# Kernel tuning notes

Measured on AMD Instinct MI355X. Metric: run time of the kernel, lower is better.

The kernel has to match this reference:

```python
import jax, jax.numpy as jnp
import numpy as np


def setup_inputs() -> dict:
    key = jax.random.key(0)
    k1, k2, k3, k4 = jax.random.split(key, 4)
    B, S, E, H = 8, 2048, 4096, 128  # batch, seq, embed, head_size
    scale = 1.0 / np.sqrt(E)
    return {
        "x": jax.random.normal(k1, (B, S, E), dtype=jnp.float32),
        "Wq": jax.random.normal(k2, (E, H), dtype=jnp.float32) * scale,
        "Wk": jax.random.normal(k3, (E, H), dtype=jnp.float32) * scale,
        "Wv": jax.random.normal(k4, (E, H), dtype=jnp.float32) * scale,
    }


def reference(x, Wq, Wk, Wv):
    # Single-head attention, non-flash branch, mask=None, eval-mode dropout.
    q = jnp.einsum("bse,eh->bsh", x, Wq)  # [B,S,H]
    k = jnp.einsum("bse,eh->bsh", x, Wk)
    v = jnp.einsum("bse,eh->bsh", x, Wv)
    head_size = k.shape[-1]
    scores = jnp.einsum("bqh,bkh->bqk", q, k) * (head_size ** -0.5)  # [B,S,S]
    attn = jax.nn.softmax(scores, axis=-1)
    out = jnp.einsum("bqk,bkh->bqh", attn, v)  # [B,S,H]
    return out
```

## Files before the change

### kernel.cpp

```cpp
#include <hip/hip_runtime.h>
#include <math.h>

typedef __bf16 bf16_t;
typedef bf16_t bf16x8 __attribute__((ext_vector_type(8)));
typedef float floatx4 __attribute__((ext_vector_type(4)));

#define MFMA(a, b, c) __builtin_amdgcn_mfma_f32_16x16x32_bf16(a, b, c, 0, 0, 0)

static constexpr int S = 2048, E = 4096, H = 128;

__device__ __forceinline__ void gl_lds16(const void* g, void* l) {
  __builtin_amdgcn_global_load_lds((const __attribute__((address_space(1))) void*)g,
                                   (__attribute__((address_space(3))) void*)l,
                                   16, 0, 0);
}

__global__ __launch_bounds__(256) void wt_kernel(const float* __restrict__ Wq,
                                                 const float* __restrict__ Wk,
                                                 const float* __restrict__ Wv,
                                                 bf16_t* __restrict__ Wt) {
  __shared__ bf16_t tile[64][130];
  int wb = blockIdx.x / 64;
  int eb = blockIdx.x % 64;
  const float* W = wb == 0 ? Wq : (wb == 1 ? Wk : Wv);
  int t = threadIdx.x;
  {
    int er = t >> 2, q = t & 3;
    const float4* src = (const float4*)(W + (size_t)(eb * 64 + er) * H + q * 32);
    for (int i = 0; i < 8; ++i) {
      float4 f = src[i];
      int c = q * 32 + i * 4;
      tile[er][c + 0] = (bf16_t)f.x; tile[er][c + 1] = (bf16_t)f.y;
      tile[er][c + 2] = (bf16_t)f.z; tile[er][c + 3] = (bf16_t)f.w;
    }
  }
  __syncthreads();
  {
    int h = t >> 1, half = t & 1;
    bf16_t buf[32];
    for (int j = 0; j < 32; ++j) buf[j] = tile[half * 32 + j][h];
    bf16_t* dst = Wt + (size_t)(wb * H + h) * E + eb * 64 + half * 32;
    for (int i = 0; i < 4; ++i) ((uint4*)dst)[i] = ((uint4*)buf)[i];
  }
}

__global__ __launch_bounds__(512, 2) void qkv_kernel(const float* __restrict__ X,
                                                     const bf16_t* __restrict__ Wt,
                                                     bf16_t* __restrict__ Qb,
                                                     bf16_t* __restrict__ Kb,
                                                     bf16_t* __restrict__ Vt) {
  __shared__ __align__(16) char smem[114688];
  constexpr int B0X = 0, B0W = 8192, B1X = 57344, B1W = 65536;

  int mBase = blockIdx.x * 64;
  int t = threadIdx.x, lane = t & 63, w = t >> 6;
  int r16 = lane & 15, q4 = lane >> 4;

  floatx4 acc[4][3] = {};

  int xrow = t >> 3;
  const float* xbase = X + (size_t)(mBase + xrow) * E + (t & 7) * 4;
  int wrl = lane >> 3, wg = lane & 7;

  floatx4 xo[2], xe[2];

#define FENCE() asm volatile("" ::: "memory")
#define WAITB(N)                                                                 \
  do {                                                                           \
    asm volatile("s_waitcnt vmcnt(" #N ") lgkmcnt(0)" ::: "memory");             \
    __builtin_amdgcn_s_barrier();                                                \
    asm volatile("" ::: "memory");                                               \
  } while (0)

#define LOAD_X(XR, K0)                                                           \
  _Pragma("unroll") for (int i = 0; i < 2; ++i)                                  \
      (XR)[i] = __builtin_nontemporal_load(                                      \
          (const floatx4*)(xbase + (K0) + i * 32));

#define STAGE_W(WOFF, K0)                                                        \
  _Pragma("unroll") for (int is = 0; is < 6; ++is) {                             \
    int row = w * 48 + is * 8 + wrl;                                             \
    int g = wg ^ (row & 7);                                                      \
    gl_lds16(Wt + (size_t)row * E + (K0) + g * 8,                                \
             smem + (WOFF) + (w * 48 + is * 8) * 128 + lane * 16);               \
  }

#define STAGE_X(XOFF, XR)                                                        \
  _Pragma("unroll") for (int i = 0; i < 2; ++i) {                                \
    floatx4 f = (XR)[i];                                                         \
    bf16_t pk[4] = {(bf16_t)f[0], (bf16_t)f[1], (bf16_t)f[2], (bf16_t)f[3]};     \
    int gc = ((t & 7) >> 1) + i * 4;                                             \
    int g = gc ^ (xrow & 7);                                                     \
    *(uint2*)(smem + (XOFF) + xrow * 128 + g * 16 + (t & 1) * 8) = *(uint2*)pk;  \
  }

#define COMPUTE(XOFF, WOFF)                                                      \
  __builtin_amdgcn_s_setprio(1);                                                 \
  _Pragma("unroll") for (int kc = 0; kc < 2; ++kc) {                             \
    bf16x8 a[4], b[3];                                                           \
    _Pragma("unroll") for (int i = 0; i < 4; ++i) {                              \
      int row = i * 16 + r16;                                                    \
      int sl = (kc * 4 + q4) ^ (row & 7);                                        \
      a[i] = *(const bf16x8*)(smem + (XOFF) + row * 128 + sl * 16);              \
    }                                                                            \
    _Pragma("unroll") for (int j = 0; j < 3; ++j) {                              \
      int row = w * 48 + j * 16 + r16;                                           \
      int sl = (kc * 4 + q4) ^ (row & 7);                                        \
      b[j] = *(const bf16x8*)(smem + (WOFF) + row * 128 + sl * 16);              \
    }                                                                            \
    _Pragma("unroll") for (int i = 0; i < 4; ++i)                                \
        _Pragma("unroll") for (int j = 0; j < 3; ++j)                            \
            acc[i][j] = MFMA(a[i], b[j], acc[i][j]);                             \
  }                                                                              \
  __builtin_amdgcn_s_setprio(0);

  LOAD_X(xe, 0);
  FENCE();
  STAGE_W(B0W, 0);
  FENCE();
  STAGE_X(B0X, xe);
  FENCE();
  LOAD_X(xo, 64);
  LOAD_X(xe, 128);
  WAITB(4);

  for (int kb = 0; kb < 62; kb += 2) {
    STAGE_W(B1W, (kb + 1) * 64);
    FENCE();
    STAGE_X(B1X, xo);
    FENCE();
    LOAD_X(xo, (kb + 3) * 64);
    FENCE();
    COMPUTE(B0X, B0W);
    WAITB(2);

    STAGE_W(B0W, (kb + 2) * 64);
    FENCE();
    STAGE_X(B0X, xe);
    FENCE();
    if (kb < 60) {
      LOAD_X(xe, (kb + 4) * 64);
      FENCE();
      COMPUTE(B1X, B1W);
      WAITB(2);
    } else {
      COMPUTE(B1X, B1W);
      WAITB(0);
    }
  }
  STAGE_W(B1W, 63 * 64);
  FENCE();
  STAGE_X(B1X, xo);
  FENCE();
  COMPUTE(B0X, B0W);
  WAITB(0);
  COMPUTE(B1X, B1W);

  int bb = mBase >> 11, sBase = mBase & 2047;
  bf16_t(*Ob)[264] = (bf16_t(*)[264])smem;
#pragma unroll
  for (int i = 0; i < 4; ++i)
#pragma unroll
    for (int j = 0; j < 3; ++j) {
      int ncol = w * 48 + j * 16;
      if (ncol >= 256) {
        int h = ncol - 256 + r16;
        bf16_t pk[4];
#pragma unroll
        for (int ii = 0; ii < 4; ++ii) pk[ii] = (bf16_t)acc[i][j][ii];
        *(uint2*)&Vt[((size_t)bb * H + h) * S + sBase + i * 16 + q4 * 4] =
            *(uint2*)pk;
      } else {
#pragma unroll
        for (int ii = 0; ii < 4; ++ii)
          Ob[i * 16 + q4 * 4 + ii][ncol + r16] = (bf16_t)acc[i][j][ii];
      }
    }
  __syncthreads();
  {
    int row = t >> 3, g = t & 7;
    bf16_t* qp = Qb + (size_t)(mBase + row) * H + g * 16;
    bf16_t* kp = Kb + (size_t)(mBase + row) * H + g * 16;
    *(uint4*)qp = *(uint4*)&Ob[row][g * 16];
    *(uint4*)(qp + 8) = *(uint4*)&Ob[row][g * 16 + 8];
    *(uint4*)kp = *(uint4*)&Ob[row][128 + g * 16];
    *(uint4*)(kp + 8) = *(uint4*)&Ob[row][128 + g * 16 + 8];
  }
#undef LOAD_X
#undef STAGE_W
#undef STAGE_X
#undef COMPUTE
#undef FENCE
#undef WAITB
}

__global__ __launch_bounds__(256, 2) void attn_kernel(const bf16_t* __restrict__ Qb,
                                                      const bf16_t* __restrict__ Kb,
                                                      const bf16_t* __restrict__ Vt,
                                                      float* __restrict__ Op,
                                                      float* __restrict__ Mp,
                                                      float* __restrict__ Lp) {
  __shared__ __align__(16) char smem[74752];

  int bid = blockIdx.x;
  int b = bid & 7, r = bid >> 3;
  int qt = r >> 1, half = r & 1;

  int t = threadIdx.x, lane = t & 63, wl = t >> 6;
  int r16 = lane & 15, q4 = lane >> 4;
  bf16_t(*Pl)[72] = (bf16_t(*)[72])(smem + 65536 + wl * 2304);

  bf16x8 qf[4];
  {
    const bf16_t* qp = Qb + (size_t)(b * S + qt * 64 + wl * 16 + r16) * H + q4 * 8;
#pragma unroll
    for (int c = 0; c < 4; ++c) qf[c] = *(const bf16x8*)(qp + c * 32);
  }
  bf16x8 onef;
#pragma unroll
  for (int i = 0; i < 8; ++i) onef[i] = (bf16_t)1.0f;

  floatx4 o[8] = {};
  float m_r[4], l_r[4];
#pragma unroll
  for (int ii = 0; ii < 4; ++ii) { m_r[ii] = -1e30f; l_r[ii] = 0.f; }
  const float scale = 0.08838834764831845f;

  int kr = lane >> 4, kg = lane & 15;
  int vr = lane >> 3, vg = lane & 7;

#define STAGE_KV(BUF, KT)                                                        \
  _Pragma("unroll") for (int is = 0; is < 4; ++is) {                             \
    int row = wl * 16 + is * 4 + kr;                                             \
    int g = kg ^ (row & 15);                                                     \
    gl_lds16(Kb + (size_t)(b * S + (KT) * 64 + row) * H + g * 8,                 \
             smem + (BUF) + (wl * 16 + is * 4) * 256 + lane * 16);               \
  }                                                                              \
  _Pragma("unroll") for (int is = 0; is < 4; ++is) {                             \
    int row = wl * 32 + is * 8 + vr;                                             \
    int g = vg ^ (row & 7);                                                      \
    gl_lds16(Vt + (size_t)(b * H + row) * S + (KT) * 64 + g * 8,                 \
             smem + (BUF) + 16384 + (wl * 32 + is * 8) * 128 + lane * 16);       \
  }

  STAGE_KV(0, half * 16);
  __syncthreads();

  for (int it = 0; it < 16; ++it) {
    int cur = (it & 1) << 15;
    if (it < 15) { STAGE_KV(cur ^ 32768, half * 16 + it + 1); }
    const char* kbase = smem + cur;
    bf16_t(*Vl)[64] = (bf16_t(*)[64])(smem + cur + 16384);

    floatx4 s4[4] = {};
    __builtin_amdgcn_s_setprio(1);
#pragma unroll
    for (int c = 0; c < 4; ++c)
#pragma unroll
      for (int j = 0; j < 4; ++j) {
        int row = j * 16 + r16;
        int sl = (c * 4 + q4) ^ r16;
        bf16x8 bk = *(const bf16x8*)(kbase + row * 256 + sl * 16);
        s4[j] = MFMA(qf[c], bk, s4[j]);
      }
    __builtin_amdgcn_s_setprio(0);

    float p[4][4], mxl[4];
#pragma unroll
    for (int ii = 0; ii < 4; ++ii) mxl[ii] = -1e30f;
#pragma unroll
    for (int j = 0; j < 4; ++j)
#pragma unroll
      for (int ii = 0; ii < 4; ++ii) {
        float sv = s4[j][ii] * scale;
        p[j][ii] = sv;
        mxl[ii] = fmaxf(mxl[ii], sv);
      }
    int ok = 1;
#pragma unroll
    for (int ii = 0; ii < 4; ++ii) ok &= (mxl[ii] <= m_r[ii] + 8.f) ? 1 : 0;
    if (!__all(ok)) {
      float alpha[4];
#pragma unroll
      for (int off = 1; off <= 8; off <<= 1)
#pragma unroll
        for (int ii = 0; ii < 4; ++ii)
          mxl[ii] = fmaxf(mxl[ii], __shfl_xor(mxl[ii], off));
#pragma unroll
      for (int ii = 0; ii < 4; ++ii) {
        float mn = fmaxf(m_r[ii], mxl[ii]);
        alpha[ii] = __expf(m_r[ii] - mn);
        m_r[ii] = mn;
        l_r[ii] *= alpha[ii];
      }
#pragma unroll
      for (int f = 0; f < 8; ++f)
#pragma unroll
        for (int ii = 0; ii < 4; ++ii) o[f][ii] *= alpha[ii];
    }
#pragma unroll
    for (int j = 0; j < 4; ++j)
#pragma unroll
      for (int ii = 0; ii < 4; ++ii) {
        float e = __expf(p[j][ii] - m_r[ii]);
        Pl[q4 * 4 + ii][j * 16 + r16] = (bf16_t)e;
      }

    bf16x8 pa0 = *(const bf16x8*)&Pl[r16][q4 * 8];
    bf16x8 pa1 = *(const bf16x8*)&Pl[r16][32 + q4 * 8];
    __builtin_amdgcn_s_setprio(1);
    floatx4 lsv = {};
    lsv = MFMA(pa0, onef, lsv);
    lsv = MFMA(pa1, onef, lsv);
#pragma unroll
    for (int f = 0; f < 8; ++f) {
      int row = f * 16 + r16;
      int sl = q4 ^ (row & 7);
      o[f] = MFMA(pa0, *(const bf16x8*)&Vl[row][sl * 8], o[f]);
    }
#pragma unroll
    for (int f = 0; f < 8; ++f) {
      int row = f * 16 + r16;
      int sl = (4 + q4) ^ (row & 7);
      o[f] = MFMA(pa1, *(const bf16x8*)&Vl[row][sl * 8], o[f]);
    }
    __builtin_amdgcn_s_setprio(0);
#pragma unroll
    for (int ii = 0; ii < 4; ++ii) l_r[ii] += lsv[ii];
    __syncthreads();
  }
#undef STAGE_KV

  int rowg = b * S + qt * 64 + wl * 16 + q4 * 4;
  float* op = Op + ((size_t)half * 16384 + rowg) * 128;
#pragma unroll
  for (int f = 0; f < 8; ++f)
#pragma unroll
    for (int ii = 0; ii < 4; ++ii)
      op[ii * 128 + f * 16 + r16] = o[f][ii];
  if (r16 == 0) {
#pragma unroll
    for (int ii = 0; ii < 4; ++ii) {
      Mp[half * 16384 + rowg + ii] = m_r[ii];
      Lp[half * 16384 + rowg + ii] = l_r[ii];
    }
  }
}

__global__ __launch_bounds__(256) void merge_kernel(const float* __restrict__ Op,
                                                    const float* __restrict__ Mp,
                                                    const float* __restrict__ Lp,
                                                    float* __restrict__ out) {
  int t = threadIdx.x;
  int row = blockIdx.x * 64 + (t >> 2);
  int c0 = (t & 3) * 32;
  float m1 = Mp[row], m2 = Mp[16384 + row];
  float l1 = Lp[row], l2 = Lp[16384 + row];
  float M = fmaxf(m1, m2);
  float e1 = __expf(m1 - M), e2 = __expf(m2 - M);
  float inv = 1.f / (e1 * l1 + e2 * l2);
  const float4* o1 = (const float4*)(Op + (size_t)row * 128 + c0);
  const float4* o2 = (const float4*)(Op + 16384ull * 128 + (size_t)row * 128 + c0);
  float4* op = (float4*)(out + (size_t)row * 128 + c0);
#pragma unroll
  for (int i = 0; i < 8; ++i) {
    float4 a = o1[i], b = o2[i];
    float4 rr;
    rr.x = (e1 * a.x + e2 * b.x) * inv;
    rr.y = (e1 * a.y + e2 * b.y) * inv;
    rr.z = (e1 * a.z + e2 * b.z) * inv;
    rr.w = (e1 * a.w + e2 * b.w) * inv;
    op[i] = rr;
  }
}

extern "C" void kernel_launch(void* const* d_in, const int* in_sizes, int n_in,
                              void* d_out, int out_size, void* d_ws, size_t ws_size,
                              hipStream_t stream) {
  const float* x = (const float*)d_in[0];
  const float* Wq = (const float*)d_in[1];
  const float* Wk = (const float*)d_in[2];
  const float* Wv = (const float*)d_in[3];
  float* out = (float*)d_out;

  bf16_t* Wt = (bf16_t*)d_ws;
  bf16_t* Qb = Wt + (size_t)384 * 4096;
  bf16_t* Kb = Qb + (size_t)16384 * 128;
  bf16_t* Vt = Kb + (size_t)16384 * 128;
  float* Op = (float*)(Vt + (size_t)8 * 128 * 2048);
  float* Mp = Op + (size_t)2 * 16384 * 128;
  float* Lp = Mp + 2 * 16384;

  wt_kernel<<<192, 256, 0, stream>>>(Wq, Wk, Wv, Wt);
  qkv_kernel<<<256, 512, 0, stream>>>(x, Wt, Qb, Kb, Vt);
  attn_kernel<<<512, 256, 0, stream>>>(Qb, Kb, Vt, Op, Mp, Lp);
  merge_kernel<<<256, 256, 0, stream>>>(Op, Mp, Lp, out);
}
```

Measured before the change: 435.3 us.

## Retile QKV projection to 256x96 blocks with XCD-aware block mapping

The QKV projection kernel now assigns each block 256 rows of X and a 96-column slice of the fused 384-column weight, instead of 64 rows by all 384 columns. Waves are arranged as a 4x2 grid over the tile. Block IDs are remapped so the four N-slices of one M group land on the same XCD, which lets the re-read X rows hit the shared L2. The trade is that each X row is loaded and converted four times, while each W tile is reused across more rows per block. The epilogue also changes, since Q and K columns can now straddle slice boundaries.

```diff
diff --git a/kernel.cpp b/kernel.cpp
--- a/kernel.cpp
+++ b/kernel.cpp
@@ -49,20 +49,27 @@
                                                      bf16_t* __restrict__ Qb,
                                                      bf16_t* __restrict__ Kb,
                                                      bf16_t* __restrict__ Vt) {
-  __shared__ __align__(16) char smem[114688];
-  constexpr int B0X = 0, B0W = 8192, B1X = 57344, B1W = 65536;
-
-  int mBase = blockIdx.x * 64;
+  __shared__ __align__(16) char smem[90112];
+  constexpr int B0X = 0, B0W = 32768, B1X = 45056, B1W = 77824;
+
+  int bid = blockIdx.x;
+  int xcd = bid & 7, idx = bid >> 3;
+  int nslice = idx & 3, mslot = idx >> 2;
+  int mgrp = mslot * 8 + xcd;
+  int mBase = mgrp * 256;
+  int nBase = nslice * 96;
+
   int t = threadIdx.x, lane = t & 63, w = t >> 6;
+  int wr = w >> 1, wc = w & 1;
   int r16 = lane & 15, q4 = lane >> 4;
 
   floatx4 acc[4][3] = {};
 
-  int xrow = t >> 3;
-  const float* xbase = X + (size_t)(mBase + xrow) * E + (t & 7) * 4;
+  int xrow = t >> 1;
+  const float* xbase = X + (size_t)(mBase + xrow) * E + (t & 1) * 4;
   int wrl = lane >> 3, wg = lane & 7;
 
-  floatx4 xo[2], xe[2];
+  floatx4 xo[8], xe[8];
 
 #define FENCE() asm volatile("" ::: "memory")
 #define WAITB(N)                                                                 \
@@ -73,24 +80,31 @@
   } while (0)
 
 #define LOAD_X(XR, K0)                                                           \
-  _Pragma("unroll") for (int i = 0; i < 2; ++i)                                  \
+  _Pragma("unroll") for (int i = 0; i < 8; ++i)                                  \
       (XR)[i] = __builtin_nontemporal_load(                                      \
-          (const floatx4*)(xbase + (K0) + i * 32));
+          (const floatx4*)(xbase + (K0) + i * 8));
 
 #define STAGE_W(WOFF, K0)                                                        \
-  _Pragma("unroll") for (int is = 0; is < 6; ++is) {                             \
-    int row = w * 48 + is * 8 + wrl;                                             \
-    int g = wg ^ (row & 7);                                                      \
-    gl_lds16(Wt + (size_t)row * E + (K0) + g * 8,                                \
-             smem + (WOFF) + (w * 48 + is * 8) * 128 + lane * 16);               \
-  }
+  do {                                                                           \
+    {                                                                            \
+      int row = w * 8 + wrl;                                                     \
+      int g = wg ^ (row & 7);                                                    \
+      gl_lds16(Wt + (size_t)(nBase + row) * E + (K0) + g * 8,                    \
+               smem + (WOFF) + (w * 8) * 128 + lane * 16);                       \
+    }                                                                            \
+    if (w < 4) {                                                                 \
+      int row = 64 + w * 8 + wrl;                                                \
+      int g = wg ^ (row & 7);                                                    \
+      gl_lds16(Wt + (size_t)(nBase + row) * E + (K0) + g * 8,                    \
+               smem + (WOFF) + (64 + w * 8) * 128 + lane * 16);                  \
+    }                                                                            \
+  } while (0)
 
 #define STAGE_X(XOFF, XR)                                                        \
-  _Pragma("unroll") for (int i = 0; i < 2; ++i) {                                \
+  _Pragma("unroll") for (int i = 0; i < 8; ++i) {                                \
     floatx4 f = (XR)[i];                                                         \
     bf16_t pk[4] = {(bf16_t)f[0], (bf16_t)f[1], (bf16_t)f[2], (bf16_t)f[3]};     \
-    int gc = ((t & 7) >> 1) + i * 4;                                             \
-    int g = gc ^ (xrow & 7);                                                     \
+    int g = i ^ (xrow & 7);                                                      \
     *(uint2*)(smem + (XOFF) + xrow * 128 + g * 16 + (t & 1) * 8) = *(uint2*)pk;  \
   }
 
@@ -99,12 +113,12 @@
   _Pragma("unroll") for (int kc = 0; kc < 2; ++kc) {                             \
     bf16x8 a[4], b[3];                                                           \
     _Pragma("unroll") for (int i = 0; i < 4; ++i) {                              \
-      int row = i * 16 + r16;                                                    \
+      int row = wr * 64 + i * 16 + r16;                                          \
       int sl = (kc * 4 + q4) ^ (row & 7);                                        \
       a[i] = *(const bf16x8*)(smem + (XOFF) + row * 128 + sl * 16);              \
     }                                                                            \
     _Pragma("unroll") for (int j = 0; j < 3; ++j) {                              \
-      int row = w * 48 + j * 16 + r16;                                           \
+      int row = wc * 48 + j * 16 + r16;                                          \
       int sl = (kc * 4 + q4) ^ (row & 7);                                        \
       b[j] = *(const bf16x8*)(smem + (WOFF) + row * 128 + sl * 16);              \
     }                                                                            \
@@ -122,7 +136,7 @@
   FENCE();
   LOAD_X(xo, 64);
   LOAD_X(xe, 128);
-  WAITB(4);
+  WAITB(16);
 
   for (int kb = 0; kb < 62; kb += 2) {
     STAGE_W(B1W, (kb + 1) * 64);
@@ -132,7 +146,7 @@
     LOAD_X(xo, (kb + 3) * 64);
     FENCE();
     COMPUTE(B0X, B0W);
-    WAITB(2);
+    WAITB(8);
 
     STAGE_W(B0W, (kb + 2) * 64);
     FENCE();
@@ -142,7 +156,7 @@
       LOAD_X(xe, (kb + 4) * 64);
       FENCE();
       COMPUTE(B1X, B1W);
-      WAITB(2);
+      WAITB(8);
     } else {
       COMPUTE(B1X, B1W);
       WAITB(0);
@@ -155,36 +169,43 @@
   COMPUTE(B0X, B0W);
   WAITB(0);
   COMPUTE(B1X, B1W);
+  __syncthreads();
 
   int bb = mBase >> 11, sBase = mBase & 2047;
-  bf16_t(*Ob)[264] = (bf16_t(*)[264])smem;
+  bf16_t(*Ob)[104] = (bf16_t(*)[104])smem;
 #pragma unroll
   for (int i = 0; i < 4; ++i)
 #pragma unroll
     for (int j = 0; j < 3; ++j) {
-      int ncol = w * 48 + j * 16;
-      if (ncol >= 256) {
-        int h = ncol - 256 + r16;
+      int lc = wc * 48 + j * 16;
+      int mrow = wr * 64 + i * 16;
+      if (nBase + lc >= 256) {
+        int h = nBase + lc - 256 + r16;
         bf16_t pk[4];
 #pragma unroll
         for (int ii = 0; ii < 4; ++ii) pk[ii] = (bf16_t)acc[i][j][ii];
-        *(uint2*)&Vt[((size_t)bb * H + h) * S + sBase + i * 16 + q4 * 4] =
+        *(uint2*)&Vt[((size_t)bb * H + h) * S + sBase + mrow + q4 * 4] =
             *(uint2*)pk;
       } else {
 #pragma unroll
         for (int ii = 0; ii < 4; ++ii)
-          Ob[i * 16 + q4 * 4 + ii][ncol + r16] = (bf16_t)acc[i][j][ii];
+          Ob[mrow + q4 * 4 + ii][lc + r16] = (bf16_t)acc[i][j][ii];
       }
     }
   __syncthreads();
   {
-    int row = t >> 3, g = t & 7;
-    bf16_t* qp = Qb + (size_t)(mBase + row) * H + g * 16;
-    bf16_t* kp = Kb + (size_t)(mBase + row) * H + g * 16;
-    *(uint4*)qp = *(uint4*)&Ob[row][g * 16];
-    *(uint4*)(qp + 8) = *(uint4*)&Ob[row][g * 16 + 8];
-    *(uint4*)kp = *(uint4*)&Ob[row][128 + g * 16];
-    *(uint4*)(kp + 8) = *(uint4*)&Ob[row][128 + g * 16 + 8];
+    int row = t >> 1, lc0 = (t & 1) * 48;
+#pragma unroll
+    for (int u = 0; u < 6; ++u) {
+      int lc = lc0 + u * 8;
+      int ncol = nBase + lc;
+      if (ncol < 256) {
+        bf16_t* dst = (ncol < 128)
+                          ? Qb + (size_t)(mBase + row) * H + ncol
+                          : Kb + (size_t)(mBase + row) * H + (ncol - 128);
+        *(uint4*)dst = *(uint4*)&Ob[row][lc];
+      }
+    }
   }
 #undef LOAD_X
 #undef STAGE_W
```

After: 623.3 us. 1.43x slower.
